# Kernel optimization log

Hardware: AMD Instinct MI355X
Metric: run time of the kernel (lower is better)

Reference implementation:

```python
import jax, jax.numpy as jnp
import numpy as np

B = 32768
Z_DIM = 64
X_DIM = 256
HIDDEN = 512
T = 8            # num_transforms
NBINS = 8
TAIL = 25.0
MULT = 3 * NBINS - 1   # widths + heights + interior derivatives = 23
MIN_W = 1e-3
MIN_H = 1e-3
MIN_D = 1e-3


def _masks():
    # MADE degrees (nflows, random_mask=False)
    d_in = np.arange(1, Z_DIM + 1)                      # input degrees 1..D
    h = np.arange(HIDDEN) % (Z_DIM - 1) + 1             # hidden degrees
    o = np.arange(Z_DIM * MULT) // MULT + 1             # output degrees, MULT contiguous per feature
    m1 = (h[:, None] >= d_in[None, :]).astype(np.float32)   # [H, D]
    m2 = (h[:, None] >= h[None, :]).astype(np.float32)      # [H, H]
    m3 = (o[:, None] > h[None, :]).astype(np.float32)       # [D*MULT, H] strict for output layer
    return jnp.asarray(m1), jnp.asarray(m2), jnp.asarray(m3)


def _rq_spline_fwd(z, uw, uh, ud):
    """Unconstrained rational-quadratic spline with linear tails (forward).
    z: [B, D]; uw/uh: [B, D, NBINS]; ud: [B, D, NBINS-1].
    Returns (outputs [B,D], logabsdet [B,D])."""
    const = np.log(np.exp(1.0 - MIN_D) - 1.0)
    pad = jnp.full(ud.shape[:-1] + (1,), const, ud.dtype)
    ud = jnp.concatenate([pad, ud, pad], axis=-1)       # [B, D, NBINS+1]

    widths = jax.nn.softmax(uw, axis=-1)
    widths = MIN_W + (1.0 - MIN_W * NBINS) * widths
    zero = jnp.zeros(widths.shape[:-1] + (1,), widths.dtype)
    cumw = jnp.concatenate([zero, jnp.cumsum(widths, axis=-1)], axis=-1)
    cumw = -TAIL + 2.0 * TAIL * cumw
    cumw = cumw.at[..., 0].set(-TAIL).at[..., -1].set(TAIL)
    widths = cumw[..., 1:] - cumw[..., :-1]

    derivs = MIN_D + jax.nn.softplus(ud)

    heights = jax.nn.softmax(uh, axis=-1)
    heights = MIN_H + (1.0 - MIN_H * NBINS) * heights
    cumh = jnp.concatenate([zero, jnp.cumsum(heights, axis=-1)], axis=-1)
    cumh = -TAIL + 2.0 * TAIL * cumh
    cumh = cumh.at[..., 0].set(-TAIL).at[..., -1].set(TAIL)
    heights = cumh[..., 1:] - cumh[..., :-1]

    delta = heights / widths

    z_in = jnp.clip(z, -TAIL, TAIL)
    edges = cumw.at[..., -1].add(1e-6)                  # nflows searchsorted eps
    idx = jnp.sum(z_in[..., None] >= edges, axis=-1) - 1
    idx = jnp.clip(idx, 0, NBINS - 1)

    g = lambda a: jnp.take_along_axis(a, idx[..., None], axis=-1)[..., 0]
    in_cw = g(cumw); in_w = g(widths)
    in_ch = g(cumh); in_h = g(heights)
    in_dl = g(delta)
    d0 = g(derivs); d1 = g(derivs[..., 1:])

    th = (z_in - in_cw) / in_w
    th1 = th * (1.0 - th)
    num = in_h * (in_dl * th * th + d0 * th1)
    den = in_dl + (d0 + d1 - 2.0 * in_dl) * th1
    out = in_ch + num / den
    dnum = in_dl ** 2 * (d1 * th * th + 2.0 * in_dl * th1 + d0 * (1.0 - th) ** 2)
    lad = jnp.log(dnum) - 2.0 * jnp.log(den)

    inside = (z >= -TAIL) & (z <= TAIL)
    return jnp.where(inside, out, z), jnp.where(inside, lad, 0.0)


def setup_inputs() -> dict:
    key = jax.random.key(0)
    ks = jax.random.split(key, 10)
    s = 0.05  # small init scale keeps spline params in a sane regime
    return {
        "z": jax.random.normal(ks[0], (B, Z_DIM), jnp.float32),
        "x": jax.random.normal(ks[1], (B, X_DIM), jnp.float32),
        "W1": jax.random.normal(ks[2], (T, HIDDEN, Z_DIM), jnp.float32) * s,
        "b1": jax.random.normal(ks[3], (T, HIDDEN), jnp.float32) * s,
        "Wc": jax.random.normal(ks[4], (T, HIDDEN, X_DIM), jnp.float32) * s,
        "bc": jax.random.normal(ks[5], (T, HIDDEN), jnp.float32) * s,
        "W2": jax.random.normal(ks[6], (T, HIDDEN, HIDDEN), jnp.float32) * s,
        "b2": jax.random.normal(ks[7], (T, HIDDEN), jnp.float32) * s,
        "W3": jax.random.normal(ks[8], (T, Z_DIM * MULT, HIDDEN), jnp.float32) * s,
        "b3": jax.random.normal(ks[9], (T, Z_DIM * MULT), jnp.float32) * s,
    }


def reference(z, x, W1, b1, Wc, bc, W2, b2, W3, b3):
    """log q(z|x) of the composed MADE-RQ-spline flow, shape [B]."""
    m1, m2, m3 = _masks()
    inv_sqrt_h = 1.0 / np.sqrt(HIDDEN)
    cur = z
    total_lad = jnp.zeros(z.shape[0], z.dtype)
    for t in range(T):
        # MADE: masked initial layer + context layer, one masked feedforward block (linear->relu), masked output layer
        h = cur @ (W1[t] * m1).T + b1[t] + x @ Wc[t].T + bc[t]
        h = jax.nn.relu(h @ (W2[t] * m2).T + b2[t])
        p = (h @ (W3[t] * m3).T + b3[t]).reshape(-1, Z_DIM, MULT)
        uw = p[..., :NBINS] * inv_sqrt_h
        uh = p[..., NBINS:2 * NBINS] * inv_sqrt_h
        ud = p[..., 2 * NBINS:]
        cur, lad = _rq_spline_fwd(cur, uw, uh, ud)
        total_lad = total_lad + lad.sum(axis=-1)
    log_base = -0.5 * jnp.sum(cur ** 2, axis=-1) - 0.5 * Z_DIM * np.log(2.0 * np.pi)
    return log_base + total_lad
```

## Files before the change

kernel.cpp:

```cpp
#include <hip/hip_runtime.h>
#include <cstdint>
#include <cstddef>

#define B_ROWS 32768
#define ZD 64
#define XD 256
#define HID 512
#define T_STEPS 8
#define MULT 23
#define MPAD 24
#define NOUT 1472
#define NPAD 1536
#define K1 320
#define PSTRIDE 200

typedef float f32x4 __attribute__((ext_vector_type(4)));
typedef short s16x8 __attribute__((ext_vector_type(8)));

__device__ __forceinline__ unsigned short f2bf(float f) {
  unsigned int u = __float_as_uint(f);
  u = (u + 0x7FFFu + ((u >> 16) & 1u)) >> 16;
  return (unsigned short)u;
}
__device__ __forceinline__ float bf2f(unsigned short s) {
  return __uint_as_float(((unsigned int)s) << 16);
}

__device__ __forceinline__ int permP(int n) {
  return (n < 72) ? (n / 9) + 63 * (n % 9)
                  : ((n - 72) >> 3) + 8 + 63 * ((n - 72) & 7);
}
__device__ __forceinline__ int degP(int n) {
  return (n < 72) ? (n / 9) + 1 : ((n - 72) >> 3) + 9;
}


__global__ void prep_weights(const float* __restrict__ W1, const float* __restrict__ Wc,
                             const float* __restrict__ W2, const float* __restrict__ W3,
                             const float* __restrict__ b1, const float* __restrict__ bc,
                             const float* __restrict__ b2, const float* __restrict__ b3,
                             unsigned short* __restrict__ w1c, unsigned short* __restrict__ w2c,
                             unsigned short* __restrict__ w3c,
                             float* __restrict__ ob1, float* __restrict__ ob2,
                             float* __restrict__ ob3) {
  const int S1 = T_STEPS * HID * K1;
  const int S2 = S1 + T_STEPS * HID * HID;
  const int S3 = S2 + T_STEPS * NPAD * HID;
  const int S4 = S3 + T_STEPS * HID;
  const int S5 = S4 + T_STEPS * HID;
  const int S6 = S5 + T_STEPS * NPAD;
  int i = blockIdx.x * 256 + threadIdx.x;
  if (i < S1) {
    int t = i / (HID * K1);
    int r = i - t * (HID * K1);
    int n = r / K1;
    int k = r - n * K1;
    int on = permP(n);
    float v;
    if (k < ZD) v = ((on % 63) >= k) ? W1[((size_t)t * HID + on) * ZD + k] : 0.0f;
    else        v = Wc[((size_t)t * HID + on) * XD + (k - ZD)];
    w1c[i] = f2bf(v);
  } else if (i < S2) {
    int j = i - S1;
    int t = j / (HID * HID);
    int r = j - t * (HID * HID);
    int n = r / HID;
    int k = r - n * HID;
    float v = 0.0f;
    if (degP(n) >= degP(k))
      v = W2[((size_t)t * HID + permP(n)) * HID + permP(k)];
    w2c[j] = f2bf(v);
  } else if (i < S3) {
    int j = i - S2;
    int t = j / (NPAD * HID);
    int r = j - t * (NPAD * HID);
    int n = r / HID;
    int k = r - n * HID;
    int d = n / MPAD;
    int jj = n - d * MPAD;
    float v = 0.0f;
    if (jj < MULT && d >= degP(k))
      v = W3[((size_t)t * NOUT + d * MULT + jj) * HID + permP(k)];
    w3c[j] = f2bf(v);
  } else if (i < S4) {
    int j = i - S3;
    int t = j / HID, n = j - t * HID;
    int on = permP(n);
    ob1[j] = b1[(size_t)t * HID + on] + bc[(size_t)t * HID + on];
  } else if (i < S5) {
    int j = i - S4;
    int t = j / HID, n = j - t * HID;
    ob2[j] = b2[(size_t)t * HID + permP(n)];
  } else if (i < S6) {
    int j = i - S5;
    int t = j / NPAD;
    int n = j - t * NPAD;
    int d = n / MPAD;
    int jj = n - d * MPAD;
    ob3[j] = (jj < MULT) ? b3[(size_t)t * NOUT + d * MULT + jj] : 0.0f;
  }
}

__global__ void prep_data(const float* __restrict__ x, const float* __restrict__ z,
                          unsigned short* __restrict__ A1,
                          float* __restrict__ curf, float* __restrict__ out) {
  const int SX = B_ROWS * XD;
  int i = blockIdx.x * 256 + threadIdx.x;
  if (i < SX) {
    int b = i >> 8;
    int j = i & 255;
    A1[(size_t)b * K1 + ZD + j] = f2bf(x[i]);
  } else {
    int j = i - SX;
    if (j < B_ROWS * ZD) {
      int b = j >> 6;
      int d = j & 63;
      float zv = z[j];
      A1[(size_t)b * K1 + d] = f2bf(zv);
      curf[j] = zv;
      if (d == 0) out[b] = -58.81206612509905f;
    }
  }
}


#define ASYNC16(gp, lp) __builtin_amdgcn_global_load_lds( \
    (__attribute__((address_space(1))) unsigned int*)(gp), \
    (__attribute__((address_space(3))) unsigned int*)(lp), 16, 0, 0)


__global__ __launch_bounds__(256, 3) void gemm_bias(
    const unsigned short* __restrict__ A,
    const unsigned short* __restrict__ Bw,
    const float* __restrict__ bias,
    unsigned short* __restrict__ C,
    int M, int N, int K, int relu, int tri)
{
  __shared__ alignas(16) unsigned short lA[2 * 128 * 32];
  __shared__ alignas(16) unsigned short lB[2 * 128 * 32];

  const int tid  = threadIdx.x;
  const int lane = tid & 63;
  const int wave = tid >> 6;

  const int lin = blockIdx.y * 4 + blockIdx.x;
  const int xcd = lin & 7;
  const int loc = lin >> 3;
  const int m0 = (xcd * 32 + (loc >> 2)) * 128;
  const int n0 = (loc & 3) * 128;
  const int Keff = tri ? min(K, 192 + n0) : K;

  const int wm = (wave >> 1) * 64;
  const int wn = (wave & 1) * 64;

  const int f    = tid * 16;
  const int row0 = f >> 6;
  const int colb = f & 63;

  char* gA0 = (char*)A  + ((size_t)(m0 + row0) * K) * 2 + colb;
  char* gA1 = gA0 + (size_t)64 * K * 2;
  char* gB0 = (char*)Bw + ((size_t)(n0 + row0) * K) * 2 + colb;
  char* gB1 = gB0 + (size_t)64 * K * 2;

  unsigned short* lA0 = lA + wave * 512;
  unsigned short* lA1 = lA + 2048 + wave * 512;
  unsigned short* lB0 = lB + wave * 512;
  unsigned short* lB1 = lB + 2048 + wave * 512;

  f32x4 acc[4][4];
#pragma unroll
  for (int i = 0; i < 4; i++)
#pragma unroll
    for (int j = 0; j < 4; j++) acc[i][j] = (f32x4){0.f, 0.f, 0.f, 0.f};

  const int fr = lane & 15;
  const int fk = (lane >> 4) * 8;

  for (int k0 = 0; k0 < Keff; k0 += 64) {
    ASYNC16(gA0, lA0);
    ASYNC16(gA1, lA1);
    ASYNC16(gB0, lB0);
    ASYNC16(gB1, lB1);
    ASYNC16(gA0 + 64, lA0 + 4096);
    ASYNC16(gA1 + 64, lA1 + 4096);
    ASYNC16(gB0 + 64, lB0 + 4096);
    ASYNC16(gB1 + 64, lB1 + 4096);
    gA0 += 128; gA1 += 128; gB0 += 128; gB1 += 128;
    __syncthreads();

    s16x8 a0[4], b0[4], a1[4], b1[4];
#pragma unroll
    for (int i = 0; i < 4; i++) {
      a0[i] = *(const s16x8*)(lA + (wm + i * 16 + fr) * 32 + fk);
      a1[i] = *(const s16x8*)(lA + 4096 + (wm + i * 16 + fr) * 32 + fk);
    }
#pragma unroll
    for (int j = 0; j < 4; j++) {
      b0[j] = *(const s16x8*)(lB + (wn + j * 16 + fr) * 32 + fk);
      b1[j] = *(const s16x8*)(lB + 4096 + (wn + j * 16 + fr) * 32 + fk);
    }

#pragma unroll
    for (int i = 0; i < 4; i++)
#pragma unroll
      for (int j = 0; j < 4; j++)
        acc[i][j] = __builtin_amdgcn_mfma_f32_16x16x32_bf16(a0[i], b0[j], acc[i][j], 0, 0, 0);
#pragma unroll
    for (int i = 0; i < 4; i++)
#pragma unroll
      for (int j = 0; j < 4; j++)
        acc[i][j] = __builtin_amdgcn_mfma_f32_16x16x32_bf16(a1[i], b1[j], acc[i][j], 0, 0, 0);
    __syncthreads();
  }

#pragma unroll
  for (int j = 0; j < 4; j++) {
    const int col = n0 + wn + j * 16 + fr;
    const float bv = bias[col];
#pragma unroll
    for (int i = 0; i < 4; i++) {
      const int rbase = m0 + wm + i * 16 + (lane >> 4) * 4;
#pragma unroll
      for (int r = 0; r < 4; r++) {
        float v = acc[i][j][r] + bv;
        if (relu) v = fmaxf(v, 0.0f);
        C[(size_t)(rbase + r) * N + col] = f2bf(v);
      }
    }
  }
}


__device__ __forceinline__ void rq_spline(const unsigned short* __restrict__ pp,
                                          float zv, float& zn, float& lad) {
  const float TAILC = 25.0f;
  const float MIN_WC = 0.001f;
  const float MIN_DC = 0.001f;
  const float SCALE2 = 0.06376007120095582f;
  const float LN2 = 0.6931471805599453f;

  s16x8 vw = *(const s16x8*)(pp);
  s16x8 vh = *(const s16x8*)(pp + 8);
  s16x8 vd = *(const s16x8*)(pp + 16);

  bool inside = (zv >= -TAILC) && (zv <= TAILC);
  float z_in = fminf(fmaxf(zv, -TAILC), TAILC);

  float ew[8], eh[8], sw = 0.f, sh = 0.f;
#pragma unroll
  for (int i = 0; i < 8; i++) {
    ew[i] = exp2f(bf2f((unsigned short)vw[i]) * SCALE2); sw += ew[i];
  }
#pragma unroll
  for (int i = 0; i < 8; i++) {
    eh[i] = exp2f(bf2f((unsigned short)vh[i]) * SCALE2); sh += eh[i];
  }
  float iw = (1.0f - 8.0f * MIN_WC) / sw;
  float ih = (1.0f - 8.0f * MIN_WC) / sh;

  float cumw[9], cumh[9];
  cumw[0] = -TAILC; cumh[0] = -TAILC;
  float cw = 0.f, ch = 0.f;
#pragma unroll
  for (int i = 0; i < 8; i++) {
    cw += MIN_WC + ew[i] * iw;
    ch += MIN_WC + eh[i] * ih;
    cumw[i + 1] = fmaf(2.0f * TAILC, cw, -TAILC);
    cumh[i + 1] = fmaf(2.0f * TAILC, ch, -TAILC);
  }
  cumw[8] = TAILC; cumh[8] = TAILC;

  int idx = 0;
#pragma unroll
  for (int i = 1; i < 8; i++) idx += (z_in >= cumw[i]) ? 1 : 0;

  float in_cw = 0.f, cw1 = 1.f, in_ch = 0.f, ch1 = 1.f, u0 = 0.f, u1 = 0.f;
#pragma unroll
  for (int i = 0; i < 8; i++) {
    if (i == idx) {
      in_cw = cumw[i]; cw1 = cumw[i + 1];
      in_ch = cumh[i]; ch1 = cumh[i + 1];
      u0 = (i > 0) ? bf2f((unsigned short)vd[i - 1]) : 0.0f;
      u1 = (i < 7) ? bf2f((unsigned short)vd[i]) : 0.0f;
    }
  }
  float dd0 = (idx == 0) ? 1.0f
            : MIN_DC + fmaxf(u0, 0.f) + __logf(1.0f + __expf(-fabsf(u0)));
  float dd1 = (idx == 7) ? 1.0f
            : MIN_DC + fmaxf(u1, 0.f) + __logf(1.0f + __expf(-fabsf(u1)));
  float in_w = cw1 - in_cw;
  float in_h = ch1 - in_ch;

  float delta = in_h / in_w;
  float th  = (z_in - in_cw) / in_w;
  float th1 = th * (1.0f - th);
  float th2 = th * th;
  float num = in_h * (delta * th2 + dd0 * th1);
  float den = delta + (dd0 + dd1 - 2.0f * delta) * th1;
  float outz = in_ch + num / den;
  float omt = 1.0f - th;
  float dnum = delta * delta * (dd1 * th2 + 2.0f * delta * th1 + dd0 * omt * omt);
  float l = LN2 * (__log2f(dnum) - 2.0f * __log2f(den));

  zn  = inside ? outz : zv;
  lad = inside ? l : 0.0f;
}


__global__ __launch_bounds__(256, 2) void gemm3_spline(
    const unsigned short* __restrict__ A,
    const unsigned short* __restrict__ Bw,
    const float* __restrict__ bias,
    float* __restrict__ curf,
    unsigned short* __restrict__ A1,
    float* __restrict__ out,
    int last)
{
  __shared__ alignas(16) union {
    unsigned short stage[2][20480];
    unsigned short p[128 * PSTRIDE];
  } sm;

  const int tid  = threadIdx.x;
  const int lane = tid & 63;
  const int wave = tid >> 6;

  const int lin = blockIdx.y * 8 + blockIdx.x;
  const int xcd = lin & 7;
  const int loc = lin >> 3;
  const int m0 = (xcd * 32 + (loc >> 3)) * 128;
  const int bn = loc & 7;
  const int n0 = bn * 192;
  const int nIter = bn + 1;

  const int wm = (wave >> 1) * 64;
  const int wn = (wave & 1) * 96;
  const int fr = lane & 15;
  const int fk = (lane >> 4) * 8;

  const int srow = tid & 127;
  const int sb = m0 + srow;
  const int dl0 = (tid >> 7) * 4;
  const int d0 = bn * 8 + dl0;
  float4 cz = *(const float4*)(curf + (size_t)sb * ZD + d0);
  float bv[6];
#pragma unroll
  for (int j = 0; j < 6; j++) bv[j] = bias[n0 + wn + j * 16 + fr];

  const int f    = tid * 16;
  const int row0 = f >> 6;
  const int colb = f & 63;
  const int K = HID;

  char* gA0 = (char*)A  + ((size_t)(m0 + row0) * K) * 2 + colb;
  char* gA1 = gA0 + (size_t)64 * K * 2;
  char* gB0 = (char*)Bw + ((size_t)(n0 + row0) * K) * 2 + colb;
  char* gB1 = gB0 + (size_t)64 * K * 2;
  char* gB2 = gB1 + (size_t)64 * K * 2;

  f32x4 acc[4][6];
#pragma unroll
  for (int i = 0; i < 4; i++)
#pragma unroll
    for (int j = 0; j < 6; j++) acc[i][j] = (f32x4){0.f, 0.f, 0.f, 0.f};

#define STAGE3(buf) do { \
    unsigned short* sa  = sm.stage[buf] + wave * 512; \
    unsigned short* sbp = sm.stage[buf] + 8192 + wave * 512; \
    ASYNC16(gA0, sa); \
    ASYNC16(gA1, sa + 2048); \
    ASYNC16(gB0, sbp); \
    ASYNC16(gB1, sbp + 2048); \
    ASYNC16(gB2, sbp + 4096); \
    ASYNC16(gA0 + 64, sa + 4096); \
    ASYNC16(gA1 + 64, sa + 6144); \
    ASYNC16(gB0 + 64, sbp + 6144); \
    ASYNC16(gB1 + 64, sbp + 8192); \
    ASYNC16(gB2 + 64, sbp + 10240); \
    gA0 += 128; gA1 += 128; gB0 += 128; gB1 += 128; gB2 += 128; \
  } while (0)

  STAGE3(0);
  __syncthreads();

  int cur = 0;
  for (int k = 0; k < nIter; ++k) {
    if (k + 1 < nIter) STAGE3(cur ^ 1);

    const unsigned short* ca = sm.stage[cur];
    const unsigned short* cb = ca + 8192;
    s16x8 a0[4], a1[4], b0[6], b1[6];
#pragma unroll
    for (int i = 0; i < 4; i++) {
      a0[i] = *(const s16x8*)(ca + (wm + i * 16 + fr) * 32 + fk);
      a1[i] = *(const s16x8*)(ca + 4096 + (wm + i * 16 + fr) * 32 + fk);
    }
#pragma unroll
    for (int j = 0; j < 6; j++) {
      b0[j] = *(const s16x8*)(cb + (wn + j * 16 + fr) * 32 + fk);
      b1[j] = *(const s16x8*)(cb + 6144 + (wn + j * 16 + fr) * 32 + fk);
    }

#pragma unroll
    for (int i = 0; i < 4; i++)
#pragma unroll
      for (int j = 0; j < 6; j++)
        acc[i][j] = __builtin_amdgcn_mfma_f32_16x16x32_bf16(a0[i], b0[j], acc[i][j], 0, 0, 0);
#pragma unroll
    for (int i = 0; i < 4; i++)
#pragma unroll
      for (int j = 0; j < 6; j++)
        acc[i][j] = __builtin_amdgcn_mfma_f32_16x16x32_bf16(a1[i], b1[j], acc[i][j], 0, 0, 0);

    __syncthreads();
    cur ^= 1;
  }
#undef STAGE3

#pragma unroll
  for (int j = 0; j < 6; j++) {
    const int col = wn + j * 16 + fr;
#pragma unroll
    for (int i = 0; i < 4; i++) {
      const int rbase = wm + i * 16 + (lane >> 4) * 4;
#pragma unroll
      for (int r = 0; r < 4; r++)
        sm.p[(rbase + r) * PSTRIDE + col] = f2bf(acc[i][j][r] + bv[j]);
    }
  }
  __syncthreads();

  const unsigned short* pp = sm.p + srow * PSTRIDE + dl0 * MPAD;
  float zn0, zn1, zn2, zn3, l0, l1, l2, l3;
  rq_spline(pp,            cz.x, zn0, l0);
  rq_spline(pp + MPAD,     cz.y, zn1, l1);
  rq_spline(pp + 2 * MPAD, cz.z, zn2, l2);
  rq_spline(pp + 3 * MPAD, cz.w, zn3, l3);

  *(float4*)(curf + (size_t)sb * ZD + d0) = make_float4(zn0, zn1, zn2, zn3);
  union { unsigned int u[2]; unsigned short s[4]; } pk;
  pk.s[0] = f2bf(zn0); pk.s[1] = f2bf(zn1); pk.s[2] = f2bf(zn2); pk.s[3] = f2bf(zn3);
  *(uint2*)(A1 + (size_t)sb * K1 + d0) = make_uint2(pk.u[0], pk.u[1]);

  float contrib = l0 + l1 + l2 + l3;
  if (last)
    contrib -= 0.5f * (zn0 * zn0 + zn1 * zn1 + zn2 * zn2 + zn3 * zn3);
  atomicAdd(&out[sb], contrib);
}


extern "C" void kernel_launch(void* const* d_in, const int* in_sizes, int n_in,
                              void* d_out, int out_size, void* d_ws, size_t ws_size,
                              hipStream_t stream)
{
  const float* z  = (const float*)d_in[0];
  const float* x  = (const float*)d_in[1];
  const float* W1 = (const float*)d_in[2];
  const float* b1 = (const float*)d_in[3];
  const float* Wc = (const float*)d_in[4];
  const float* bc = (const float*)d_in[5];
  const float* W2 = (const float*)d_in[6];
  const float* b2 = (const float*)d_in[7];
  const float* W3 = (const float*)d_in[8];
  const float* b3 = (const float*)d_in[9];
  float* out = (float*)d_out;
  char* ws = (char*)d_ws;

  size_t oA1 = 0;
  size_t oH1 = oA1 + (size_t)B_ROWS * K1 * 2;
  size_t oH2 = oH1 + (size_t)B_ROWS * HID * 2;
  size_t oCU = oH2 + (size_t)B_ROWS * HID * 2;
  size_t oW1 = oCU + (size_t)B_ROWS * ZD * 4;
  size_t oW2 = oW1 + (size_t)T_STEPS * HID * K1 * 2;
  size_t oW3 = oW2 + (size_t)T_STEPS * HID * HID * 2;
  size_t oB1 = oW3 + (size_t)T_STEPS * NPAD * HID * 2;
  size_t oB2 = oB1 + (size_t)T_STEPS * HID * 4;
  size_t oB3 = oB2 + (size_t)T_STEPS * HID * 4;

  unsigned short* A1  = (unsigned short*)(ws + oA1);
  unsigned short* h1  = (unsigned short*)(ws + oH1);
  unsigned short* h2  = (unsigned short*)(ws + oH2);
  float* curf = (float*)(ws + oCU);
  unsigned short* w1c = (unsigned short*)(ws + oW1);
  unsigned short* w2c = (unsigned short*)(ws + oW2);
  unsigned short* w3c = (unsigned short*)(ws + oW3);
  float* b1c = (float*)(ws + oB1);
  float* b2p = (float*)(ws + oB2);
  float* b3c = (float*)(ws + oB3);

  const int prepw_total = T_STEPS * (HID * K1 + HID * HID + NPAD * HID + 2 * HID + NPAD);
  prep_weights<<<(prepw_total + 255) / 256, 256, 0, stream>>>(
      W1, Wc, W2, W3, b1, bc, b2, b3, w1c, w2c, w3c, b1c, b2p, b3c);
  const int prepd_total = B_ROWS * (XD + ZD);
  prep_data<<<(prepd_total + 255) / 256, 256, 0, stream>>>(x, z, A1, curf, out);

  for (int t = 0; t < T_STEPS; ++t) {
    gemm_bias<<<dim3(4, B_ROWS / 128), 256, 0, stream>>>(
        A1, w1c + (size_t)t * HID * K1, b1c + (size_t)t * HID, h1,
        B_ROWS, HID, K1, 0, 0);
    gemm_bias<<<dim3(4, B_ROWS / 128), 256, 0, stream>>>(
        h1, w2c + (size_t)t * HID * HID, b2p + (size_t)t * HID, h2,
        B_ROWS, HID, HID, 1, 1);
    gemm3_spline<<<dim3(8, B_ROWS / 128), 256, 0, stream>>>(
        h2, w3c + (size_t)t * NPAD * HID, b3c + (size_t)t * NPAD,
        curf, A1, out, (t == T_STEPS - 1) ? 1 : 0);
  }
}
```

Measured before the change: 1.001 ms.

## Triple-buffer K-loop with async LDS prefetch and explicit vmcnt waits in both GEMMs

Both GEMM kernels now stage K-slices of 32 instead of 64 into a three-deep LDS ring and prefetch two stages ahead. Explicit s_waitcnt vmcnt counts and raw s_barrier calls replace the full __syncthreads drains. gemm_bias previously had no prefetch at all, so global loads were fully exposed; the change lets those loads overlap the MFMA work. In exchange it doubles the number of loop iterations and barriers, and it relies on hand-set wait counts being correct.

```diff
diff --git a/kernel.cpp b/kernel.cpp
--- a/kernel.cpp
+++ b/kernel.cpp
@@ -128,6 +128,8 @@
     (__attribute__((address_space(1))) unsigned int*)(gp), \
     (__attribute__((address_space(3))) unsigned int*)(lp), 16, 0, 0)
 
+#define WAITV(n) asm volatile("s_waitcnt vmcnt(" #n ")" ::: "memory")
+
 
 __global__ __launch_bounds__(256, 3) void gemm_bias(
     const unsigned short* __restrict__ A,
@@ -136,8 +138,7 @@
     unsigned short* __restrict__ C,
     int M, int N, int K, int relu, int tri)
 {
-  __shared__ alignas(16) unsigned short lA[2 * 128 * 32];
-  __shared__ alignas(16) unsigned short lB[2 * 128 * 32];
+  __shared__ alignas(16) unsigned short lS[3][8192];
 
   const int tid  = threadIdx.x;
   const int lane = tid & 63;
@@ -149,6 +150,7 @@
   const int m0 = (xcd * 32 + (loc >> 2)) * 128;
   const int n0 = (loc & 3) * 128;
   const int Keff = tri ? min(K, 192 + n0) : K;
+  const int nIter = Keff >> 5;
 
   const int wm = (wave >> 1) * 64;
   const int wn = (wave & 1) * 64;
@@ -162,11 +164,6 @@
   char* gB0 = (char*)Bw + ((size_t)(n0 + row0) * K) * 2 + colb;
   char* gB1 = gB0 + (size_t)64 * K * 2;
 
-  unsigned short* lA0 = lA + wave * 512;
-  unsigned short* lA1 = lA + 2048 + wave * 512;
-  unsigned short* lB0 = lB + wave * 512;
-  unsigned short* lB1 = lB + 2048 + wave * 512;
-
   f32x4 acc[4][4];
 #pragma unroll
   for (int i = 0; i < 4; i++)
@@ -176,42 +173,47 @@
   const int fr = lane & 15;
   const int fk = (lane >> 4) * 8;
 
-  for (int k0 = 0; k0 < Keff; k0 += 64) {
-    ASYNC16(gA0, lA0);
-    ASYNC16(gA1, lA1);
-    ASYNC16(gB0, lB0);
-    ASYNC16(gB1, lB1);
-    ASYNC16(gA0 + 64, lA0 + 4096);
-    ASYNC16(gA1 + 64, lA1 + 4096);
-    ASYNC16(gB0 + 64, lB0 + 4096);
-    ASYNC16(gB1 + 64, lB1 + 4096);
-    gA0 += 128; gA1 += 128; gB0 += 128; gB1 += 128;
-    __syncthreads();
-
-    s16x8 a0[4], b0[4], a1[4], b1[4];
-#pragma unroll
-    for (int i = 0; i < 4; i++) {
-      a0[i] = *(const s16x8*)(lA + (wm + i * 16 + fr) * 32 + fk);
-      a1[i] = *(const s16x8*)(lA + 4096 + (wm + i * 16 + fr) * 32 + fk);
-    }
-#pragma unroll
-    for (int j = 0; j < 4; j++) {
-      b0[j] = *(const s16x8*)(lB + (wn + j * 16 + fr) * 32 + fk);
-      b1[j] = *(const s16x8*)(lB + 4096 + (wn + j * 16 + fr) * 32 + fk);
-    }
-
+#define STAGEB(sp) do { \
+    unsigned short* s_ = (sp) + wave * 512; \
+    ASYNC16(gA0, s_); \
+    ASYNC16(gA1, s_ + 2048); \
+    ASYNC16(gB0, s_ + 4096); \
+    ASYNC16(gB1, s_ + 6144); \
+    gA0 += 64; gA1 += 64; gB0 += 64; gB1 += 64; \
+  } while (0)
+
+  STAGEB(lS[0]);
+  STAGEB(lS[1]);
+
+  for (int k = 0; k < nIter; ++k) {
+    __builtin_amdgcn_sched_barrier(0);
+    if (k + 2 < nIter) STAGEB(lS[0] + ((k + 2) % 3) * 8192);
+    const int nv = nIter - 1 - k;
+    if (nv >= 2)      WAITV(8);
+    else if (nv == 1) WAITV(4);
+    else              WAITV(0);
+    __builtin_amdgcn_s_barrier();
+    __builtin_amdgcn_sched_barrier(0);
+
+    const unsigned short* cs = lS[0] + (k % 3) * 8192;
+    s16x8 a[4], b[4];
 #pragma unroll
     for (int i = 0; i < 4; i++)
+      a[i] = *(const s16x8*)(cs + (wm + i * 16 + fr) * 32 + fk);
+#pragma unroll
+    for (int j = 0; j < 4; j++)
+      b[j] = *(const s16x8*)(cs + 4096 + (wn + j * 16 + fr) * 32 + fk);
+
+#pragma unroll
+    for (int i = 0; i < 4; i++)
 #pragma unroll
       for (int j = 0; j < 4; j++)
-        acc[i][j] = __builtin_amdgcn_mfma_f32_16x16x32_bf16(a0[i], b0[j], acc[i][j], 0, 0, 0);
-#pragma unroll
-    for (int i = 0; i < 4; i++)
-#pragma unroll
-      for (int j = 0; j < 4; j++)
-        acc[i][j] = __builtin_amdgcn_mfma_f32_16x16x32_bf16(a1[i], b1[j], acc[i][j], 0, 0, 0);
-    __syncthreads();
-  }
+        acc[i][j] = __builtin_amdgcn_mfma_f32_16x16x32_bf16(a[i], b[j], acc[i][j], 0, 0, 0);
+
+    __builtin_amdgcn_sched_barrier(0);
+    __builtin_amdgcn_s_barrier();
+  }
+#undef STAGEB
 
 #pragma unroll
   for (int j = 0; j < 4; j++) {
@@ -317,7 +319,7 @@
     int last)
 {
   __shared__ alignas(16) union {
-    unsigned short stage[2][20480];
+    unsigned short stage[3][10240];
     unsigned short p[128 * PSTRIDE];
   } sm;
 
@@ -331,7 +333,7 @@
   const int m0 = (xcd * 32 + (loc >> 3)) * 128;
   const int bn = loc & 7;
   const int n0 = bn * 192;
-  const int nIter = bn + 1;
+  const int nIter = 2 * (bn + 1);
 
   const int wm = (wave >> 1) * 64;
   const int wn = (wave & 1) * 96;
@@ -364,56 +366,46 @@
 #pragma unroll
     for (int j = 0; j < 6; j++) acc[i][j] = (f32x4){0.f, 0.f, 0.f, 0.f};
 
-#define STAGE3(buf) do { \
-    unsigned short* sa  = sm.stage[buf] + wave * 512; \
-    unsigned short* sbp = sm.stage[buf] + 8192 + wave * 512; \
-    ASYNC16(gA0, sa); \
-    ASYNC16(gA1, sa + 2048); \
-    ASYNC16(gB0, sbp); \
-    ASYNC16(gB1, sbp + 2048); \
-    ASYNC16(gB2, sbp + 4096); \
-    ASYNC16(gA0 + 64, sa + 4096); \
-    ASYNC16(gA1 + 64, sa + 6144); \
-    ASYNC16(gB0 + 64, sbp + 6144); \
-    ASYNC16(gB1 + 64, sbp + 8192); \
-    ASYNC16(gB2 + 64, sbp + 10240); \
-    gA0 += 128; gA1 += 128; gB0 += 128; gB1 += 128; gB2 += 128; \
+#define STAGE3(sp) do { \
+    unsigned short* s_ = (sp) + wave * 512; \
+    ASYNC16(gA0, s_); \
+    ASYNC16(gA1, s_ + 2048); \
+    ASYNC16(gB0, s_ + 4096); \
+    ASYNC16(gB1, s_ + 6144); \
+    ASYNC16(gB2, s_ + 8192); \
+    gA0 += 64; gA1 += 64; gB0 += 64; gB1 += 64; gB2 += 64; \
   } while (0)
 
-  STAGE3(0);
-  __syncthreads();
-
-  int cur = 0;
+  STAGE3(sm.stage[0]);
+  STAGE3(sm.stage[1]);
+
   for (int k = 0; k < nIter; ++k) {
-    if (k + 1 < nIter) STAGE3(cur ^ 1);
-
-    const unsigned short* ca = sm.stage[cur];
-    const unsigned short* cb = ca + 8192;
-    s16x8 a0[4], a1[4], b0[6], b1[6];
-#pragma unroll
-    for (int i = 0; i < 4; i++) {
-      a0[i] = *(const s16x8*)(ca + (wm + i * 16 + fr) * 32 + fk);
-      a1[i] = *(const s16x8*)(ca + 4096 + (wm + i * 16 + fr) * 32 + fk);
-    }
-#pragma unroll
-    for (int j = 0; j < 6; j++) {
-      b0[j] = *(const s16x8*)(cb + (wn + j * 16 + fr) * 32 + fk);
-      b1[j] = *(const s16x8*)(cb + 6144 + (wn + j * 16 + fr) * 32 + fk);
-    }
-
+    __builtin_amdgcn_sched_barrier(0);
+    if (k + 2 < nIter) STAGE3(sm.stage[0] + ((k + 2) % 3) * 10240);
+    const int nv = nIter - 1 - k;
+    if (nv >= 2)      WAITV(10);
+    else if (nv == 1) WAITV(5);
+    else              WAITV(0);
+    __builtin_amdgcn_s_barrier();
+    __builtin_amdgcn_sched_barrier(0);
+
+    const unsigned short* cs = sm.stage[0] + (k % 3) * 10240;
+    s16x8 a[4], b[6];
 #pragma unroll
     for (int i = 0; i < 4; i++)
+      a[i] = *(const s16x8*)(cs + (wm + i * 16 + fr) * 32 + fk);
+#pragma unroll
+    for (int j = 0; j < 6; j++)
+      b[j] = *(const s16x8*)(cs + 4096 + (wn + j * 16 + fr) * 32 + fk);
+
+#pragma unroll
+    for (int i = 0; i < 4; i++)
 #pragma unroll
       for (int j = 0; j < 6; j++)
-        acc[i][j] = __builtin_amdgcn_mfma_f32_16x16x32_bf16(a0[i], b0[j], acc[i][j], 0, 0, 0);
-#pragma unroll
-    for (int i = 0; i < 4; i++)
-#pragma unroll
-      for (int j = 0; j < 6; j++)
-        acc[i][j] = __builtin_amdgcn_mfma_f32_16x16x32_bf16(a1[i], b1[j], acc[i][j], 0, 0, 0);
-
-    __syncthreads();
-    cur ^= 1;
+        acc[i][j] = __builtin_amdgcn_mfma_f32_16x16x32_bf16(a[i], b[j], acc[i][j], 0, 0, 0);
+
+    __builtin_amdgcn_sched_barrier(0);
+    __builtin_amdgcn_s_barrier();
   }
 #undef STAGE3
 
```

New measurement: 1.045 ms. +4.3%, slower.
